# Kernel optimization log

Hardware: AMD Instinct MI355X
Metric: run time of the kernel (lower is better)

Reference implementation:

```python
import jax, jax.numpy as jnp
import numpy as np

EMBED_DIM = 1024
NUM_HEADS = 16
HEAD_DIM = EMBED_DIM // NUM_HEADS
SCALE = HEAD_DIM ** -0.5
EPS = 1e-5


def layer_norm(x, gamma, beta):
    mu = jnp.mean(x, axis=-1, keepdims=True)
    var = jnp.var(x, axis=-1, keepdims=True)
    return (x - mu) * jax.lax.rsqrt(var + EPS) * gamma + beta


def setup_inputs() -> dict:
    key = jax.random.key(0)
    ks = jax.random.split(key, 12)
    d = EMBED_DIM
    xav = (6.0 / (d + d)) ** 0.5
    x = jax.random.normal(ks[0], (4, 1024, d), dtype=jnp.float32)
    Wq = jax.random.uniform(ks[1], (d, d), jnp.float32, -xav, xav)
    Wk = jax.random.uniform(ks[2], (d, d), jnp.float32, -xav, xav)
    Wv = jax.random.uniform(ks[3], (d, d), jnp.float32, -xav, xav)
    Wo = jax.random.uniform(ks[4], (d, d), jnp.float32, -xav, xav)
    bq = jnp.zeros((d,), jnp.float32)
    bk = jnp.zeros((d,), jnp.float32)
    bv = jnp.zeros((d,), jnp.float32)
    bo = jnp.zeros((d,), jnp.float32)
    ones = jnp.ones((d,), jnp.float32)
    zeros = jnp.zeros((d,), jnp.float32)
    return {
        "x": x,
        "Wq": Wq, "bq": bq, "Wk": Wk, "bk": bk, "Wv": Wv, "bv": bv,
        "Wo": Wo, "bo": bo,
        "qn_g": ones, "qn_b": zeros,
        "kn_g": ones, "kn_b": zeros,
        "vn_g": ones, "vn_b": zeros,
        "on_g": ones, "on_b": zeros,
    }


def reference(x, Wq, bq, Wk, bk, Wv, bv, Wo, bo,
              qn_g, qn_b, kn_g, kn_b, vn_g, vn_b, on_g, on_b):
    B, S, D = x.shape
    H, Hd = NUM_HEADS, HEAD_DIM
    # projections (nn.Linear: x @ W.T + b) followed by LayerNorm
    Q = layer_norm(x @ Wq.T + bq, qn_g, qn_b) * SCALE
    K = layer_norm(x @ Wk.T + bk, kn_g, kn_b)
    V = layer_norm(x @ Wv.T + bv, vn_g, vn_b)
    Q = Q.reshape(B, S, H, Hd).transpose(0, 2, 1, 3)  # [B,H,S,Hd]
    K = K.reshape(B, S, H, Hd).transpose(0, 2, 1, 3)
    V = V.reshape(B, S, H, Hd).transpose(0, 2, 1, 3)
    scores = jnp.einsum('bhqd,bhkd->bhqk', Q, K)
    scores = jnp.clip(scores, -10.0, 10.0)
    attn = jax.nn.softmax(scores, axis=-1)  # dropout = identity at eval
    out = jnp.einsum('bhqk,bhkd->bhqd', attn, V)
    out = out.transpose(0, 2, 1, 3).reshape(B, S, D)
    out = out @ Wo.T + bo
    return layer_norm(out, on_g, on_b)
```

## Files before the change

kernel.cpp:

```cpp
#include <hip/hip_runtime.h>
#include <stdint.h>
#include <stddef.h>

typedef unsigned short u16;
typedef __bf16 bf16x8 __attribute__((ext_vector_type(8)));
typedef float f32x4 __attribute__((ext_vector_type(4)));
typedef u16 u16x8 __attribute__((ext_vector_type(8)));

#define SEQ    1024
#define DEMB   1024
#define MROWS  4096
#define NHEAD  16
#define HD     64
#define QSCALE 0.125f
#define LN_EPS 1e-5f

static __device__ __forceinline__ u16 f2bf(float f) {
  union { float f; unsigned u; } c; c.f = f;
  unsigned r = c.u + 0x7FFFu + ((c.u >> 16) & 1u);
  return (u16)(r >> 16);
}
static __device__ __forceinline__ float bf2f(unsigned h) {
  union { unsigned u; float f; } c; c.u = h << 16; return c.f;
}

static __device__ __forceinline__ void gload16(const void* g, void* l) {
  __builtin_amdgcn_global_load_lds((const __attribute__((address_space(1))) void*)g,
                                   (__attribute__((address_space(3))) void*)l, 16, 0, 0);
}

__global__ void cvt_kernel(const float* __restrict__ x,
                           const float* __restrict__ wq, const float* __restrict__ wk,
                           const float* __restrict__ wv, const float* __restrict__ wo,
                           u16* __restrict__ xb, u16* __restrict__ wb) {
  size_t e = ((size_t)blockIdx.x * blockDim.x + threadIdx.x) * 8;
  const float* src; u16* dst; size_t off;
  if (e < (size_t)MROWS * DEMB) { src = x; dst = xb; off = e; }
  else {
    size_t we = e - (size_t)MROWS * DEMB;
    int plane = (int)(we >> 20);
    src = (plane == 0) ? wq : (plane == 1) ? wk : (plane == 2) ? wv : wo;
    dst = wb + ((size_t)plane << 20);
    off = we & ((1u << 20) - 1);
  }
  float4 a = *(const float4*)(src + off);
  float4 b = *(const float4*)(src + off + 4);
  u16 o[8] = { f2bf(a.x), f2bf(a.y), f2bf(a.z), f2bf(a.w),
               f2bf(b.x), f2bf(b.y), f2bf(b.z), f2bf(b.w) };
  uint4 pk;
  pk.x = (unsigned)o[0] | ((unsigned)o[1] << 16);
  pk.y = (unsigned)o[2] | ((unsigned)o[3] << 16);
  pk.z = (unsigned)o[4] | ((unsigned)o[5] << 16);
  pk.w = (unsigned)o[6] | ((unsigned)o[7] << 16);
  *(uint4*)(dst + off) = pk;
}

__global__ __launch_bounds__(256)
void gemm_bt(const u16* __restrict__ A, const u16* __restrict__ B0,
             const u16* __restrict__ B1, const u16* __restrict__ B2,
             u16* __restrict__ C, int M, int N, int K) {
  __shared__ u16 lA[128 * 32];
  __shared__ u16 lB[128 * 32];
  const u16* Bp = (blockIdx.z == 0) ? B0 : (blockIdx.z == 1) ? B1 : B2;
  u16* Cp = C + (size_t)blockIdx.z * ((size_t)M * N);
  const int tid = threadIdx.x;
  const int w = tid >> 6, l = tid & 63;
  const int lr = l & 15, lg = l >> 4;
  const int m0 = blockIdx.x * 128, n0 = blockIdx.y * 128;
  const int wm = (w & 1) * 64, wn = (w >> 1) * 64;
  f32x4 acc[4][4] = {};
  const int cid0 = w * 64 + l;
  const int cid1 = 256 + w * 64 + l;
  const int rowA0 = cid0 >> 2, kc0 = (cid0 & 3) * 8;
  const int rowA1 = cid1 >> 2, kc1 = (cid1 & 3) * 8;
  for (int kt = 0; kt < K; kt += 32) {
    __syncthreads();
    gload16(A  + (size_t)(m0 + rowA0) * K + kt + kc0, lA + (size_t)(w * 64) * 8);
    gload16(A  + (size_t)(m0 + rowA1) * K + kt + kc1, lA + (size_t)(256 + w * 64) * 8);
    gload16(Bp + (size_t)(n0 + rowA0) * K + kt + kc0, lB + (size_t)(w * 64) * 8);
    gload16(Bp + (size_t)(n0 + rowA1) * K + kt + kc1, lB + (size_t)(256 + w * 64) * 8);
    __syncthreads();
    bf16x8 af[4], bfg[4];
#pragma unroll
    for (int mb = 0; mb < 4; ++mb)
      af[mb] = *(const bf16x8*)(lA + (wm + mb * 16 + lr) * 32 + lg * 8);
#pragma unroll
    for (int nb = 0; nb < 4; ++nb)
      bfg[nb] = *(const bf16x8*)(lB + (wn + nb * 16 + lr) * 32 + lg * 8);
#pragma unroll
    for (int mb = 0; mb < 4; ++mb)
#pragma unroll
      for (int nb = 0; nb < 4; ++nb)
        acc[mb][nb] = __builtin_amdgcn_mfma_f32_16x16x32_bf16(af[mb], bfg[nb], acc[mb][nb], 0, 0, 0);
  }
#pragma unroll
  for (int mb = 0; mb < 4; ++mb)
#pragma unroll
    for (int nb = 0; nb < 4; ++nb)
#pragma unroll
      for (int r = 0; r < 4; ++r) {
        int row = m0 + wm + mb * 16 + lg * 4 + r;
        int col = n0 + wn + nb * 16 + lr;
        Cp[(size_t)row * N + col] = f2bf(acc[mb][nb][r]);
      }
}

static __device__ __forceinline__ void block_reduce2(float& s1, float& s2, float* red) {
#pragma unroll
  for (int o = 32; o > 0; o >>= 1) { s1 += __shfl_xor(s1, o); s2 += __shfl_xor(s2, o); }
  int w = threadIdx.x >> 6, l = threadIdx.x & 63;
  if (l == 0) { red[w * 2] = s1; red[w * 2 + 1] = s2; }
  __syncthreads();
  s1 = red[0] + red[2] + red[4] + red[6];
  s2 = red[1] + red[3] + red[5] + red[7];
}

__global__ void ln_qkv_kernel(const u16* __restrict__ projb,
                              const float* __restrict__ bq, const float* __restrict__ bk,
                              const float* __restrict__ bv,
                              const float* __restrict__ qg, const float* __restrict__ qb,
                              const float* __restrict__ kg, const float* __restrict__ kb,
                              const float* __restrict__ vg, const float* __restrict__ vb,
                              u16* __restrict__ Qh, u16* __restrict__ Kh, u16* __restrict__ Vh) {
  __shared__ float red[8];
  const int row = blockIdx.x & (MROWS - 1);
  const int plane = blockIdx.x >> 12;
  const float* bias; const float* gam; const float* bet; u16* op; float scl;
  if (plane == 0)      { bias = bq; gam = qg; bet = qb; op = Qh; scl = QSCALE; }
  else if (plane == 1) { bias = bk; gam = kg; bet = kb; op = Kh; scl = 1.f; }
  else                 { bias = bv; gam = vg; bet = vb; op = Vh; scl = 1.f; }
  const u16* src = projb + ((size_t)plane * MROWS + row) * DEMB;
  const int t = threadIdx.x;
  uint2 pv = *(const uint2*)(src + t * 4);
  float4 v;
  v.x = bf2f(pv.x & 0xffffu); v.y = bf2f(pv.x >> 16);
  v.z = bf2f(pv.y & 0xffffu); v.w = bf2f(pv.y >> 16);
  float4 bz = *(const float4*)(bias + t * 4);
  v.x += bz.x; v.y += bz.y; v.z += bz.z; v.w += bz.w;
  float s1 = v.x + v.y + v.z + v.w;
  float s2 = v.x * v.x + v.y * v.y + v.z * v.z + v.w * v.w;
  block_reduce2(s1, s2, red);
  const float mean = s1 * (1.f / DEMB);
  const float var = s2 * (1.f / DEMB) - mean * mean;
  const float rstd = rsqrtf(var + LN_EPS);
  float4 gg = *(const float4*)(gam + t * 4);
  float4 bb = *(const float4*)(bet + t * 4);
  u16 o0 = f2bf(((v.x - mean) * rstd * gg.x + bb.x) * scl);
  u16 o1 = f2bf(((v.y - mean) * rstd * gg.y + bb.y) * scl);
  u16 o2 = f2bf(((v.z - mean) * rstd * gg.z + bb.z) * scl);
  u16 o3 = f2bf(((v.w - mean) * rstd * gg.w + bb.w) * scl);
  const int b = row >> 10, s = row & (SEQ - 1);
  const int h = t >> 4;
  u16* dst = op + ((size_t)(b * NHEAD + h) * SEQ + s) * HD + (t & 15) * 4;
  uint2 pk;
  pk.x = (unsigned)o0 | ((unsigned)o1 << 16);
  pk.y = (unsigned)o2 | ((unsigned)o3 << 16);
  *(uint2*)dst = pk;
}

__global__ __launch_bounds__(256)
void vtr_kernel(const u16* __restrict__ Vtmp, u16* __restrict__ VT) {
  __shared__ u16 t[64][72];
  const int stile = blockIdx.x & 15, bh = blockIdx.x >> 4;
  const u16* src = Vtmp + ((size_t)bh * SEQ + stile * 64) * HD;
  const int tid = threadIdx.x;
  {
    const int c0 = tid * 2;
    const int r = c0 >> 3, c = c0 & 7;
    uint4 v0 = *(const uint4*)(src + (size_t)r * HD + c * 8);
    uint4 v1 = *(const uint4*)(src + (size_t)r * HD + (c + 1) * 8);
    *(uint4*)&t[r][c * 8] = v0;
    *(uint4*)&t[r][(c + 1) * 8] = v1;
  }
  __syncthreads();
  const int d = tid >> 2, sc = tid & 3;
  u16 buf[16];
#pragma unroll
  for (int j = 0; j < 16; ++j) buf[j] = t[sc * 16 + j][d];
  u16* dst = VT + ((size_t)bh * HD + d) * SEQ + stile * 64 + sc * 16;
  *(uint4*)(dst)     = *(uint4*)&buf[0];
  *(uint4*)(dst + 8) = *(uint4*)&buf[8];
}

__global__ __launch_bounds__(64)
void attn_kernel(const u16* __restrict__ Qh, const u16* __restrict__ Kh,
                 const u16* __restrict__ VT, u16* __restrict__ AO) {
  __shared__ u16 Pt[32][76];
  const int bid = blockIdx.x;
  const int wg = (bid & 7) * 256 + (bid >> 3);
  const int qt = wg & 31, bh = wg >> 5;
  const int b = bh >> 4, h = bh & 15;
  const u16* Qp = Qh + (size_t)bh * SEQ * HD;
  const u16* Kp = Kh + (size_t)bh * SEQ * HD;
  const u16* Vp = VT + (size_t)bh * HD * SEQ;
  const int l = threadIdx.x;
  const int lr = l & 15, lg = l >> 4;
  bf16x8 qa[2][2];
#pragma unroll
  for (int m = 0; m < 2; ++m) {
    const u16* qr = Qp + (size_t)(qt * 32 + m * 16 + lr) * HD + lg * 8;
    qa[m][0] = *(const bf16x8*)qr;
    qa[m][1] = *(const bf16x8*)(qr + 32);
  }
  f32x4 o[2][4] = {};
  float rs[2][4] = {{0.f,0.f,0.f,0.f},{0.f,0.f,0.f,0.f}};
  for (int kt = 0; kt < SEQ / 64; ++kt) {
    f32x4 sv[2][4];
#pragma unroll
    for (int kb = 0; kb < 4; ++kb) {
      const u16* kr = Kp + (size_t)(kt * 64 + kb * 16 + lr) * HD + lg * 8;
      bf16x8 k0 = *(const bf16x8*)kr;
      bf16x8 k1 = *(const bf16x8*)(kr + 32);
#pragma unroll
      for (int m = 0; m < 2; ++m) {
        f32x4 s0 = {};
        s0 = __builtin_amdgcn_mfma_f32_16x16x32_bf16(qa[m][0], k0, s0, 0, 0, 0);
        s0 = __builtin_amdgcn_mfma_f32_16x16x32_bf16(qa[m][1], k1, s0, 0, 0, 0);
        sv[m][kb] = s0;
      }
    }
#pragma unroll
    for (int m = 0; m < 2; ++m)
#pragma unroll
      for (int kb = 0; kb < 4; ++kb)
#pragma unroll
        for (int r = 0; r < 4; ++r) {
          float xx = fminf(10.f, fmaxf(-10.f, sv[m][kb][r]));
          float p = exp2f(xx * 1.4426950408889634f);
          rs[m][r] += p;
          Pt[m * 16 + lg * 4 + r][kb * 16 + lr] = f2bf(p);
        }
    bf16x8 pa[2][2];
#pragma unroll
    for (int m = 0; m < 2; ++m) {
      pa[m][0] = *(const bf16x8*)&Pt[m * 16 + lr][lg * 8];
      pa[m][1] = *(const bf16x8*)&Pt[m * 16 + lr][32 + lg * 8];
    }
#pragma unroll
    for (int nb = 0; nb < 4; ++nb) {
      const u16* vr = Vp + (size_t)(nb * 16 + lr) * SEQ + kt * 64 + lg * 8;
      bf16x8 v0 = *(const bf16x8*)vr;
      bf16x8 v1 = *(const bf16x8*)(vr + 32);
#pragma unroll
      for (int m = 0; m < 2; ++m) {
        o[m][nb] = __builtin_amdgcn_mfma_f32_16x16x32_bf16(pa[m][0], v0, o[m][nb], 0, 0, 0);
        o[m][nb] = __builtin_amdgcn_mfma_f32_16x16x32_bf16(pa[m][1], v1, o[m][nb], 0, 0, 0);
      }
    }
  }
#pragma unroll
  for (int m = 0; m < 2; ++m)
#pragma unroll
    for (int r = 0; r < 4; ++r) {
      float vsum = rs[m][r];
      vsum += __shfl_xor(vsum, 1);
      vsum += __shfl_xor(vsum, 2);
      vsum += __shfl_xor(vsum, 4);
      vsum += __shfl_xor(vsum, 8);
      rs[m][r] = vsum;
    }
#pragma unroll
  for (int m = 0; m < 2; ++m)
#pragma unroll
    for (int nb = 0; nb < 4; ++nb)
#pragma unroll
      for (int r = 0; r < 4; ++r) {
        const int srow = qt * 32 + m * 16 + lg * 4 + r;
        const int col = h * HD + nb * 16 + lr;
        AO[((size_t)b * SEQ + srow) * DEMB + col] = f2bf(o[m][nb][r] / rs[m][r]);
      }
}

__global__ void ln_out_kernel(const u16* __restrict__ src0, const float* __restrict__ bo,
                              const float* __restrict__ og, const float* __restrict__ ob,
                              float* __restrict__ out) {
  __shared__ float red[8];
  const int row = blockIdx.x;
  const u16* src = src0 + (size_t)row * DEMB;
  const int t = threadIdx.x;
  uint2 pv = *(const uint2*)(src + t * 4);
  float4 v;
  v.x = bf2f(pv.x & 0xffffu); v.y = bf2f(pv.x >> 16);
  v.z = bf2f(pv.y & 0xffffu); v.w = bf2f(pv.y >> 16);
  float4 bz = *(const float4*)(bo + t * 4);
  v.x += bz.x; v.y += bz.y; v.z += bz.z; v.w += bz.w;
  float s1 = v.x + v.y + v.z + v.w;
  float s2 = v.x * v.x + v.y * v.y + v.z * v.z + v.w * v.w;
  block_reduce2(s1, s2, red);
  const float mean = s1 * (1.f / DEMB);
  const float var = s2 * (1.f / DEMB) - mean * mean;
  const float rstd = rsqrtf(var + LN_EPS);
  float4 gg = *(const float4*)(og + t * 4);
  float4 bb = *(const float4*)(ob + t * 4);
  float4 r;
  r.x = (v.x - mean) * rstd * gg.x + bb.x;
  r.y = (v.y - mean) * rstd * gg.y + bb.y;
  r.z = (v.z - mean) * rstd * gg.z + bb.z;
  r.w = (v.w - mean) * rstd * gg.w + bb.w;
  *(float4*)(out + (size_t)row * DEMB + t * 4) = r;
}

extern "C" void kernel_launch(void* const* d_in, const int* in_sizes, int n_in,
                              void* d_out, int out_size, void* d_ws, size_t ws_size,
                              hipStream_t stream) {
  (void)in_sizes; (void)n_in; (void)out_size; (void)ws_size;
  const float* x  = (const float*)d_in[0];
  const float* Wq = (const float*)d_in[1];
  const float* bq = (const float*)d_in[2];
  const float* Wk = (const float*)d_in[3];
  const float* bk = (const float*)d_in[4];
  const float* Wv = (const float*)d_in[5];
  const float* bv = (const float*)d_in[6];
  const float* Wo = (const float*)d_in[7];
  const float* bo = (const float*)d_in[8];
  const float* qg = (const float*)d_in[9];
  const float* qb = (const float*)d_in[10];
  const float* kg = (const float*)d_in[11];
  const float* kb = (const float*)d_in[12];
  const float* vg = (const float*)d_in[13];
  const float* vb = (const float*)d_in[14];
  const float* og = (const float*)d_in[15];
  const float* ob = (const float*)d_in[16];

  char* ws = (char*)d_ws;
  u16* xb    = (u16*)(ws);
  u16* wb    = (u16*)(ws + ((size_t)8  << 20));
  u16* projb = (u16*)(ws + ((size_t)16 << 20));
  u16* Qh    = (u16*)(ws + ((size_t)40 << 20));
  u16* Kh    = (u16*)(ws + ((size_t)48 << 20));
  u16* VT    = (u16*)(ws + ((size_t)56 << 20));
  u16* Vtmp  = xb;
  u16* AOp   = xb;
  u16* oprojb = projb;

  cvt_kernel<<<4096, 256, 0, stream>>>(x, Wq, Wk, Wv, Wo, xb, wb);

  dim3 gqkv(32, 8, 3);
  gemm_bt<<<gqkv, 256, 0, stream>>>(xb, wb, wb + (1u << 20), wb + (2u << 20),
                                    projb, MROWS, DEMB, DEMB);

  ln_qkv_kernel<<<3 * MROWS, 256, 0, stream>>>(projb, bq, bk, bv,
                                               qg, qb, kg, kb, vg, vb,
                                               Qh, Kh, Vtmp);

  vtr_kernel<<<1024, 256, 0, stream>>>(Vtmp, VT);

  attn_kernel<<<2048, 64, 0, stream>>>(Qh, Kh, VT, AOp);

  dim3 go(32, 8, 1);
  gemm_bt<<<go, 256, 0, stream>>>(AOp, wb + (3u << 20), wb + (3u << 20), wb + (3u << 20),
                                  oprojb, MROWS, DEMB, DEMB);

  ln_out_kernel<<<MROWS, 256, 0, stream>>>(oprojb, bo, og, ob, (float*)d_out);
}
```

Before: 262.1 us.

## Split attention key range across two waves with LDS combine

The attention kernel now runs two waves per block, each handling half of the key sequence with its own P staging buffer, and the partial outputs and row sums are merged through shared memory before the final normalization. K and V fragments are loaded into registers ahead of the MFMAs, and scheduling barriers are placed between phases. The aim is more parallelism and latency hiding per query tile, at the cost of extra LDS and a block-level sync and combine step. The GEMM loads were also rewritten with union casts, which does not change the work done.

```diff
diff --git a/kernel.cpp b/kernel.cpp
--- a/kernel.cpp
+++ b/kernel.cpp
@@ -27,6 +27,11 @@
 static __device__ __forceinline__ void gload16(const void* g, void* l) {
   __builtin_amdgcn_global_load_lds((const __attribute__((address_space(1))) void*)g,
                                    (__attribute__((address_space(3))) void*)l, 16, 0, 0);
+}
+
+static __device__ __forceinline__ void mem_fence_sched() {
+  asm volatile("" ::: "memory");
+  __builtin_amdgcn_sched_barrier(0);
 }
 
 __global__ void cvt_kernel(const float* __restrict__ x,
@@ -82,11 +87,17 @@
     __syncthreads();
     bf16x8 af[4], bfg[4];
 #pragma unroll
-    for (int mb = 0; mb < 4; ++mb)
-      af[mb] = *(const bf16x8*)(lA + (wm + mb * 16 + lr) * 32 + lg * 8);
-#pragma unroll
-    for (int nb = 0; nb < 4; ++nb)
-      bfg[nb] = *(const bf16x8*)(lB + (wn + nb * 16 + lr) * 32 + lg * 8);
+    for (int mb = 0; mb < 4; ++mb) {
+      union { u16x8 u; bf16x8 v; } cv;
+      cv.u = *(const u16x8*)(lA + (wm + mb * 16 + lr) * 32 + lg * 8);
+      af[mb] = cv.v;
+    }
+#pragma unroll
+    for (int nb = 0; nb < 4; ++nb) {
+      union { u16x8 u; bf16x8 v; } cv;
+      cv.u = *(const u16x8*)(lB + (wn + nb * 16 + lr) * 32 + lg * 8);
+      bfg[nb] = cv.v;
+    }
 #pragma unroll
     for (int mb = 0; mb < 4; ++mb)
 #pragma unroll
@@ -182,10 +193,12 @@
   *(uint4*)(dst + 8) = *(uint4*)&buf[8];
 }
 
-__global__ __launch_bounds__(64)
+__global__ __launch_bounds__(128)
 void attn_kernel(const u16* __restrict__ Qh, const u16* __restrict__ Kh,
                  const u16* __restrict__ VT, u16* __restrict__ AO) {
-  __shared__ u16 Pt[32][76];
+  __shared__ u16 Pt[2][32][76];
+  __shared__ float oL[32][64];
+  __shared__ float rsL[32];
   const int bid = blockIdx.x;
   const int wg = (bid & 7) * 256 + (bid >> 3);
   const int qt = wg & 31, bh = wg >> 5;
@@ -193,60 +206,78 @@
   const u16* Qp = Qh + (size_t)bh * SEQ * HD;
   const u16* Kp = Kh + (size_t)bh * SEQ * HD;
   const u16* Vp = VT + (size_t)bh * HD * SEQ;
-  const int l = threadIdx.x;
+  const int tid = threadIdx.x, w = tid >> 6, l = tid & 63;
   const int lr = l & 15, lg = l >> 4;
   bf16x8 qa[2][2];
 #pragma unroll
   for (int m = 0; m < 2; ++m) {
     const u16* qr = Qp + (size_t)(qt * 32 + m * 16 + lr) * HD + lg * 8;
-    qa[m][0] = *(const bf16x8*)qr;
-    qa[m][1] = *(const bf16x8*)(qr + 32);
+    union { u16x8 u; bf16x8 v; } c0, c1;
+    c0.u = *(const u16x8*)qr;
+    c1.u = *(const u16x8*)(qr + 32);
+    qa[m][0] = c0.v; qa[m][1] = c1.v;
   }
   f32x4 o[2][4] = {};
   float rs[2][4] = {{0.f,0.f,0.f,0.f},{0.f,0.f,0.f,0.f}};
-  for (int kt = 0; kt < SEQ / 64; ++kt) {
-    f32x4 sv[2][4];
+  const int kbase = w * (SEQ / 2);
+  for (int t = 0; t < 8; ++t) {
+    const int k0 = kbase + t * 64;
+    bf16x8 kf[4][2];
 #pragma unroll
     for (int kb = 0; kb < 4; ++kb) {
-      const u16* kr = Kp + (size_t)(kt * 64 + kb * 16 + lr) * HD + lg * 8;
-      bf16x8 k0 = *(const bf16x8*)kr;
-      bf16x8 k1 = *(const bf16x8*)(kr + 32);
-#pragma unroll
-      for (int m = 0; m < 2; ++m) {
+      const u16* kr = Kp + (size_t)(k0 + kb * 16 + lr) * HD + lg * 8;
+      union { u16x8 u; bf16x8 v; } c0, c1;
+      c0.u = *(const u16x8*)kr;
+      c1.u = *(const u16x8*)(kr + 32);
+      kf[kb][0] = c0.v; kf[kb][1] = c1.v;
+    }
+#pragma unroll
+    for (int m = 0; m < 2; ++m) {
+      f32x4 sv[4];
+#pragma unroll
+      for (int kb = 0; kb < 4; ++kb) {
         f32x4 s0 = {};
-        s0 = __builtin_amdgcn_mfma_f32_16x16x32_bf16(qa[m][0], k0, s0, 0, 0, 0);
-        s0 = __builtin_amdgcn_mfma_f32_16x16x32_bf16(qa[m][1], k1, s0, 0, 0, 0);
-        sv[m][kb] = s0;
+        s0 = __builtin_amdgcn_mfma_f32_16x16x32_bf16(qa[m][0], kf[kb][0], s0, 0, 0, 0);
+        s0 = __builtin_amdgcn_mfma_f32_16x16x32_bf16(qa[m][1], kf[kb][1], s0, 0, 0, 0);
+        sv[kb] = s0;
       }
-    }
-#pragma unroll
-    for (int m = 0; m < 2; ++m)
 #pragma unroll
       for (int kb = 0; kb < 4; ++kb)
 #pragma unroll
         for (int r = 0; r < 4; ++r) {
-          float xx = fminf(10.f, fmaxf(-10.f, sv[m][kb][r]));
+          float xx = fminf(10.f, fmaxf(-10.f, sv[kb][r]));
           float p = exp2f(xx * 1.4426950408889634f);
           rs[m][r] += p;
-          Pt[m * 16 + lg * 4 + r][kb * 16 + lr] = f2bf(p);
+          Pt[w][m * 16 + lg * 4 + r][kb * 16 + lr] = f2bf(p);
         }
+    }
+    mem_fence_sched();
+    bf16x8 vf[4][2];
+#pragma unroll
+    for (int nb = 0; nb < 4; ++nb) {
+      const u16* vr = Vp + (size_t)(nb * 16 + lr) * SEQ + k0 + lg * 8;
+      union { u16x8 u; bf16x8 v; } c0, c1;
+      c0.u = *(const u16x8*)vr;
+      c1.u = *(const u16x8*)(vr + 32);
+      vf[nb][0] = c0.v; vf[nb][1] = c1.v;
+    }
     bf16x8 pa[2][2];
 #pragma unroll
-    for (int m = 0; m < 2; ++m) {
-      pa[m][0] = *(const bf16x8*)&Pt[m * 16 + lr][lg * 8];
-      pa[m][1] = *(const bf16x8*)&Pt[m * 16 + lr][32 + lg * 8];
-    }
-#pragma unroll
-    for (int nb = 0; nb < 4; ++nb) {
-      const u16* vr = Vp + (size_t)(nb * 16 + lr) * SEQ + kt * 64 + lg * 8;
-      bf16x8 v0 = *(const bf16x8*)vr;
-      bf16x8 v1 = *(const bf16x8*)(vr + 32);
+    for (int m = 0; m < 2; ++m)
+#pragma unroll
+      for (int h2 = 0; h2 < 2; ++h2) {
+        union { u16x8 u; bf16x8 v; } cv;
+        cv.u = *(const u16x8*)&Pt[w][m * 16 + lr][h2 * 32 + lg * 8];
+        pa[m][h2] = cv.v;
+      }
+#pragma unroll
+    for (int nb = 0; nb < 4; ++nb)
 #pragma unroll
       for (int m = 0; m < 2; ++m) {
-        o[m][nb] = __builtin_amdgcn_mfma_f32_16x16x32_bf16(pa[m][0], v0, o[m][nb], 0, 0, 0);
-        o[m][nb] = __builtin_amdgcn_mfma_f32_16x16x32_bf16(pa[m][1], v1, o[m][nb], 0, 0, 0);
+        o[m][nb] = __builtin_amdgcn_mfma_f32_16x16x32_bf16(pa[m][0], vf[nb][0], o[m][nb], 0, 0, 0);
+        o[m][nb] = __builtin_amdgcn_mfma_f32_16x16x32_bf16(pa[m][1], vf[nb][1], o[m][nb], 0, 0, 0);
       }
-    }
+    mem_fence_sched();
   }
 #pragma unroll
   for (int m = 0; m < 2; ++m)
@@ -259,16 +290,38 @@
       vsum += __shfl_xor(vsum, 8);
       rs[m][r] = vsum;
     }
-#pragma unroll
-  for (int m = 0; m < 2; ++m)
-#pragma unroll
-    for (int nb = 0; nb < 4; ++nb)
+  if (w == 1) {
+#pragma unroll
+    for (int m = 0; m < 2; ++m)
+#pragma unroll
+      for (int nb = 0; nb < 4; ++nb)
+#pragma unroll
+        for (int r = 0; r < 4; ++r)
+          oL[m * 16 + lg * 4 + r][nb * 16 + lr] = o[m][nb][r];
+    if (lr == 0) {
+#pragma unroll
+      for (int m = 0; m < 2; ++m)
+#pragma unroll
+        for (int r = 0; r < 4; ++r)
+          rsL[m * 16 + lg * 4 + r] = rs[m][r];
+    }
+  }
+  __syncthreads();
+  if (w == 0) {
+#pragma unroll
+    for (int m = 0; m < 2; ++m)
 #pragma unroll
       for (int r = 0; r < 4; ++r) {
-        const int srow = qt * 32 + m * 16 + lg * 4 + r;
-        const int col = h * HD + nb * 16 + lr;
-        AO[((size_t)b * SEQ + srow) * DEMB + col] = f2bf(o[m][nb][r] / rs[m][r]);
+        const int row = m * 16 + lg * 4 + r;
+        const float inv = 1.f / (rs[m][r] + rsL[row]);
+        const int srow = qt * 32 + row;
+#pragma unroll
+        for (int nb = 0; nb < 4; ++nb) {
+          float tot = (o[m][nb][r] + oL[row][nb * 16 + lr]) * inv;
+          AO[((size_t)b * SEQ + srow) * DEMB + h * HD + nb * 16 + lr] = f2bf(tot);
+        }
       }
+  }
 }
 
 __global__ void ln_out_kernel(const u16* __restrict__ src0, const float* __restrict__ bo,
@@ -345,7 +398,7 @@
 
   vtr_kernel<<<1024, 256, 0, stream>>>(Vtmp, VT);
 
-  attn_kernel<<<2048, 64, 0, stream>>>(Qh, Kh, VT, AOp);
+  attn_kernel<<<2048, 128, 0, stream>>>(Qh, Kh, VT, AOp);
 
   dim3 go(32, 8, 1);
   gemm_bt<<<go, 256, 0, stream>>>(AOp, wb + (3u << 20), wb + (3u << 20), wb + (3u << 20),
```

Result: faster. 252.5 us (-3.7%).

## Rewrite attention with 32x32 MFMA, permlane P transpose, and split-K across two waves

Applied to the files above, without the earlier changes.

The attention kernel now computes S^T with 32x32x16 MFMAs, so each lane holds whole query columns. The probability tile is rearranged into the A-operand layout with permlane32_swap instead of a round trip through shared memory. The key range is split across two waves per block, and their partial outputs and row sums are combined through LDS at the end. This removes the per-tile LDS write, read and sync for P and doubles the waves per block, at the cost of a final cross-wave reduction in which only one wave stores the output.

```diff
diff --git a/kernel.cpp b/kernel.cpp
--- a/kernel.cpp
+++ b/kernel.cpp
@@ -5,7 +5,9 @@
 typedef unsigned short u16;
 typedef __bf16 bf16x8 __attribute__((ext_vector_type(8)));
 typedef float f32x4 __attribute__((ext_vector_type(4)));
+typedef float f32x16 __attribute__((ext_vector_type(16)));
 typedef u16 u16x8 __attribute__((ext_vector_type(8)));
+typedef unsigned uint32x2 __attribute__((ext_vector_type(2)));
 
 #define SEQ    1024
 #define DEMB   1024
@@ -22,6 +24,10 @@
 }
 static __device__ __forceinline__ float bf2f(unsigned h) {
   union { unsigned u; float f; } c; c.u = h << 16; return c.f;
+}
+static __device__ __forceinline__ unsigned pack2bf(float a, float b) {
+  union { __bf16 h; u16 u; } x, y; x.h = (__bf16)a; y.h = (__bf16)b;
+  return (unsigned)x.u | ((unsigned)y.u << 16);
 }
 
 static __device__ __forceinline__ void gload16(const void* g, void* l) {
@@ -82,11 +88,17 @@
     __syncthreads();
     bf16x8 af[4], bfg[4];
 #pragma unroll
-    for (int mb = 0; mb < 4; ++mb)
-      af[mb] = *(const bf16x8*)(lA + (wm + mb * 16 + lr) * 32 + lg * 8);
-#pragma unroll
-    for (int nb = 0; nb < 4; ++nb)
-      bfg[nb] = *(const bf16x8*)(lB + (wn + nb * 16 + lr) * 32 + lg * 8);
+    for (int mb = 0; mb < 4; ++mb) {
+      union { u16x8 u; bf16x8 v; } cv;
+      cv.u = *(const u16x8*)(lA + (wm + mb * 16 + lr) * 32 + lg * 8);
+      af[mb] = cv.v;
+    }
+#pragma unroll
+    for (int nb = 0; nb < 4; ++nb) {
+      union { u16x8 u; bf16x8 v; } cv;
+      cv.u = *(const u16x8*)(lB + (wn + nb * 16 + lr) * 32 + lg * 8);
+      bfg[nb] = cv.v;
+    }
 #pragma unroll
     for (int mb = 0; mb < 4; ++mb)
 #pragma unroll
@@ -182,10 +194,11 @@
   *(uint4*)(dst + 8) = *(uint4*)&buf[8];
 }
 
-__global__ __launch_bounds__(64)
+__global__ __launch_bounds__(128)
 void attn_kernel(const u16* __restrict__ Qh, const u16* __restrict__ Kh,
                  const u16* __restrict__ VT, u16* __restrict__ AO) {
-  __shared__ u16 Pt[32][76];
+  __shared__ float oL[32][64];
+  __shared__ float rsL[32];
   const int bid = blockIdx.x;
   const int wg = (bid & 7) * 256 + (bid >> 3);
   const int qt = wg & 31, bh = wg >> 5;
@@ -193,82 +206,81 @@
   const u16* Qp = Qh + (size_t)bh * SEQ * HD;
   const u16* Kp = Kh + (size_t)bh * SEQ * HD;
   const u16* Vp = VT + (size_t)bh * HD * SEQ;
-  const int l = threadIdx.x;
-  const int lr = l & 15, lg = l >> 4;
-  bf16x8 qa[2][2];
-#pragma unroll
-  for (int m = 0; m < 2; ++m) {
-    const u16* qr = Qp + (size_t)(qt * 32 + m * 16 + lr) * HD + lg * 8;
-    qa[m][0] = *(const bf16x8*)qr;
-    qa[m][1] = *(const bf16x8*)(qr + 32);
-  }
-  f32x4 o[2][4] = {};
-  float rs[2][4] = {{0.f,0.f,0.f,0.f},{0.f,0.f,0.f,0.f}};
-  for (int kt = 0; kt < SEQ / 64; ++kt) {
-    f32x4 sv[2][4];
-#pragma unroll
-    for (int kb = 0; kb < 4; ++kb) {
-      const u16* kr = Kp + (size_t)(kt * 64 + kb * 16 + lr) * HD + lg * 8;
-      bf16x8 k0 = *(const bf16x8*)kr;
-      bf16x8 k1 = *(const bf16x8*)(kr + 32);
-#pragma unroll
-      for (int m = 0; m < 2; ++m) {
-        f32x4 s0 = {};
-        s0 = __builtin_amdgcn_mfma_f32_16x16x32_bf16(qa[m][0], k0, s0, 0, 0, 0);
-        s0 = __builtin_amdgcn_mfma_f32_16x16x32_bf16(qa[m][1], k1, s0, 0, 0, 0);
-        sv[m][kb] = s0;
+  const int tid = threadIdx.x, w = tid >> 6, l = tid & 63;
+  const int q = l & 31, hi = l >> 5;
+  bf16x8 qf[4];
+#pragma unroll
+  for (int dt = 0; dt < 4; ++dt) {
+    union { u16x8 u; bf16x8 v; } cv;
+    cv.u = *(const u16x8*)(Qp + (size_t)(qt * 32 + q) * HD + dt * 16 + hi * 8);
+    qf[dt] = cv.v;
+  }
+  f32x16 o0 = {}, o1 = {};
+  float rs = 0.f;
+  const int kbase = w * (SEQ / 2);
+  for (int t = 0; t < 8; ++t) {
+    const int k0 = kbase + t * 64;
+    unsigned W[2][8];
+#pragma unroll
+    for (int kc = 0; kc < 2; ++kc) {
+      f32x16 sc = {};
+#pragma unroll
+      for (int dt = 0; dt < 4; ++dt) {
+        union { u16x8 u; bf16x8 v; } cv;
+        cv.u = *(const u16x8*)(Kp + (size_t)(k0 + kc * 32 + q) * HD + dt * 16 + hi * 8);
+        sc = __builtin_amdgcn_mfma_f32_32x32x16_bf16(cv.v, qf[dt], sc, 0, 0, 0);
       }
-    }
-#pragma unroll
-    for (int m = 0; m < 2; ++m)
-#pragma unroll
-      for (int kb = 0; kb < 4; ++kb)
-#pragma unroll
-        for (int r = 0; r < 4; ++r) {
-          float xx = fminf(10.f, fmaxf(-10.f, sv[m][kb][r]));
-          float p = exp2f(xx * 1.4426950408889634f);
-          rs[m][r] += p;
-          Pt[m * 16 + lg * 4 + r][kb * 16 + lr] = f2bf(p);
-        }
-    bf16x8 pa[2][2];
-#pragma unroll
-    for (int m = 0; m < 2; ++m) {
-      pa[m][0] = *(const bf16x8*)&Pt[m * 16 + lr][lg * 8];
-      pa[m][1] = *(const bf16x8*)&Pt[m * 16 + lr][32 + lg * 8];
-    }
-#pragma unroll
-    for (int nb = 0; nb < 4; ++nb) {
-      const u16* vr = Vp + (size_t)(nb * 16 + lr) * SEQ + kt * 64 + lg * 8;
-      bf16x8 v0 = *(const bf16x8*)vr;
-      bf16x8 v1 = *(const bf16x8*)(vr + 32);
-#pragma unroll
-      for (int m = 0; m < 2; ++m) {
-        o[m][nb] = __builtin_amdgcn_mfma_f32_16x16x32_bf16(pa[m][0], v0, o[m][nb], 0, 0, 0);
-        o[m][nb] = __builtin_amdgcn_mfma_f32_16x16x32_bf16(pa[m][1], v1, o[m][nb], 0, 0, 0);
+      float pv[16];
+#pragma unroll
+      for (int r = 0; r < 16; ++r) {
+        float xx = fminf(10.f, fmaxf(-10.f, sc[r]));
+        float p = exp2f(xx * 1.4426950408889634f);
+        rs += p;
+        pv[r] = p;
       }
-    }
-  }
-#pragma unroll
-  for (int m = 0; m < 2; ++m)
-#pragma unroll
-    for (int r = 0; r < 4; ++r) {
-      float vsum = rs[m][r];
-      vsum += __shfl_xor(vsum, 1);
-      vsum += __shfl_xor(vsum, 2);
-      vsum += __shfl_xor(vsum, 4);
-      vsum += __shfl_xor(vsum, 8);
-      rs[m][r] = vsum;
-    }
-#pragma unroll
-  for (int m = 0; m < 2; ++m)
-#pragma unroll
-    for (int nb = 0; nb < 4; ++nb)
-#pragma unroll
-      for (int r = 0; r < 4; ++r) {
-        const int srow = qt * 32 + m * 16 + lg * 4 + r;
-        const int col = h * HD + nb * 16 + lr;
-        AO[((size_t)b * SEQ + srow) * DEMB + col] = f2bf(o[m][nb][r] / rs[m][r]);
+#pragma unroll
+      for (int i = 0; i < 8; ++i)
+        W[kc][i] = pack2bf(pv[2 * i], pv[2 * i + 1]);
+    }
+#pragma unroll
+    for (int kt = 0; kt < 4; ++kt) {
+      const int kcx = kt >> 1, ktl = kt & 1;
+      uint32x2 s0 = __builtin_amdgcn_permlane32_swap(W[kcx][4 * ktl + 0], W[kcx][4 * ktl + 2], false, false);
+      uint32x2 s1 = __builtin_amdgcn_permlane32_swap(W[kcx][4 * ktl + 1], W[kcx][4 * ktl + 3], false, false);
+      union { unsigned u[4]; bf16x8 v; } pa;
+      pa.u[0] = s0[0]; pa.u[1] = s1[0]; pa.u[2] = s0[1]; pa.u[3] = s1[1];
+      {
+        union { u16x8 u; bf16x8 v; } v0, v1;
+        v0.u = *(const u16x8*)(Vp + (size_t)(0 * 32 + q) * SEQ + k0 + kt * 16 + hi * 8);
+        v1.u = *(const u16x8*)(Vp + (size_t)(1 * 32 + q) * SEQ + k0 + kt * 16 + hi * 8);
+        o0 = __builtin_amdgcn_mfma_f32_32x32x16_bf16(pa.v, v0.v, o0, 0, 0, 0);
+        o1 = __builtin_amdgcn_mfma_f32_32x32x16_bf16(pa.v, v1.v, o1, 0, 0, 0);
       }
+    }
+  }
+  rs += __shfl_xor(rs, 32);
+  if (w == 1) {
+#pragma unroll
+    for (int r = 0; r < 16; ++r) {
+      const int row = (r & 3) + 8 * (r >> 2) + 4 * hi;
+      oL[row][q]      = o0[r];
+      oL[row][32 + q] = o1[r];
+    }
+    if (hi == 0) rsL[q] = rs;
+  }
+  __syncthreads();
+  if (w == 0) {
+    const float inv_q = 1.f / (rs + rsL[q]);
+#pragma unroll
+    for (int r = 0; r < 16; ++r) {
+      const int row = (r & 3) + 8 * (r >> 2) + 4 * hi;
+      const float invr = __shfl(inv_q, row);
+      const int srow = qt * 32 + row;
+      const size_t base = ((size_t)b * SEQ + srow) * DEMB + h * HD;
+      AO[base + q]      = f2bf((o0[r] + oL[row][q]) * invr);
+      AO[base + 32 + q] = f2bf((o1[r] + oL[row][32 + q]) * invr);
+    }
+  }
 }
 
 __global__ void ln_out_kernel(const u16* __restrict__ src0, const float* __restrict__ bo,
@@ -345,7 +357,7 @@
 
   vtr_kernel<<<1024, 256, 0, stream>>>(Vtmp, VT);
 
-  attn_kernel<<<2048, 64, 0, stream>>>(Qh, Kh, VT, AOp);
+  attn_kernel<<<2048, 128, 0, stream>>>(Qh, Kh, VT, AOp);
 
   dim3 go(32, 8, 1);
   gemm_bt<<<go, 256, 0, stream>>>(AOp, wb + (3u << 20), wb + (3u << 20), wb + (3u << 20),
```

Measured after the change: 256.8 us. -2.0%, faster.
